# Kernel tuning notes

Measured on AMD Instinct MI355X. Metric: run time of the kernel, lower is better.

Reference implementation:

```python
import jax, jax.numpy as jnp
import numpy as np

N_QUBITS = 6
DIM = 2 ** N_QUBITS  # 64
Q_LAYERS = 2
CHUNK = 16

# ---- single-qubit rotation gate matrices (batched over leading dim) ----

def _rx(t):
    c = jnp.cos(t / 2).astype(jnp.complex64)
    s = jnp.sin(t / 2).astype(jnp.complex64)
    return jnp.stack([jnp.stack([c, -1j * s], -1), jnp.stack([-1j * s, c], -1)], -2)

def _ry(t):
    c = jnp.cos(t / 2).astype(jnp.complex64)
    s = jnp.sin(t / 2).astype(jnp.complex64)
    return jnp.stack([jnp.stack([c, -s], -1), jnp.stack([s, c], -1)], -2)

def _rz(t):
    e = jnp.exp(-0.5j * t.astype(jnp.complex64))
    z = jnp.zeros_like(e)
    return jnp.stack([jnp.stack([e, z], -1), jnp.stack([z, jnp.conj(e)], -1)], -2)


def _apply_1q(state, gate, wire):
    # state: (B, 64) complex64; gate: (B,2,2). PennyLane wire 0 = most-significant bit.
    dl, dr = 2 ** wire, 2 ** (N_QUBITS - 1 - wire)
    s = state.reshape(-1, dl, 2, dr)
    s = jnp.einsum('bkj,bljr->blkr', gate, s)
    return s.reshape(-1, DIM)


def _apply_crx(state, theta, control, target):
    s = state.reshape((-1,) + (2,) * N_QUBITS)
    s = jnp.moveaxis(s, (control + 1, target + 1), (1, 2))
    g = _rx(theta)  # (B,2,2)
    s1 = jnp.einsum('bkj,bj...->bk...', g, s[:, 1])
    s = jnp.concatenate([s[:, :1], s1[:, None]], axis=1)
    s = jnp.moveaxis(s, (1, 2), (control + 1, target + 1))
    return s.reshape(-1, DIM)


def _ansatz(state, params, n_layers):
    # unified ansatz: per layer, RX/RY/RZ on each qubit, ring of CRX forward, ring of CRX backward
    idx = 0
    for _ in range(n_layers):
        for i in range(N_QUBITS):
            state = _apply_1q(state, _rx(params[:, idx]), i)
            state = _apply_1q(state, _ry(params[:, idx + 1]), i)
            state = _apply_1q(state, _rz(params[:, idx + 2]), i)
            idx += 3
        for i in range(N_QUBITS):
            state = _apply_crx(state, params[:, idx], i, (i + 1) % N_QUBITS)
            idx += 1
        for i in range(N_QUBITS - 1, -1, -1):
            state = _apply_crx(state, params[:, idx], i, (i - 1) % N_QUBITS)
            idx += 1
    return state


_PX = jnp.array([[0, 1], [1, 0]], jnp.complex64)
_PY = jnp.array([[0, -1j], [1j, 0]], jnp.complex64)
_PZ = jnp.array([[1, 0], [0, -1]], jnp.complex64)


def _expvals(state):
    # expectations of X_i, Y_i, Z_i for all qubits -> (B, 3*n_qubits)
    outs = []
    B = state.shape[0]
    for P in (_PX, _PY, _PZ):
        g = jnp.broadcast_to(P, (B, 2, 2))
        for i in range(N_QUBITS):
            ps = _apply_1q(state, g, i)
            outs.append(jnp.sum(jnp.conj(state) * ps, axis=1).real)
    return jnp.stack(outs, axis=1).astype(jnp.float32)


def _forward(x, emb_w, emb_b, att_w1, att_b1, att_w2, att_b2, proj_w, proj_b,
             mix_re, mix_im, qff_params, out_w, out_b, ln_g, ln_b,
             cls_w1, cls_b1, cls_w2, cls_b2):
    B, C, T = x.shape
    # classical feature extractor: (B,C,T) -> (B,T,D)
    feats = jnp.einsum('bct,cd->btd', x, emb_w) + emb_b
    D = feats.shape[-1]
    n_chunks = T // CHUNK
    xc = feats.reshape(B, n_chunks, CHUNK, D)
    # attention-weighted chunk aggregation
    h = jnp.tanh(xc @ att_w1 + att_b1)
    scores = h @ att_w2 + att_b2                      # (B,nc,CHUNK,1)
    w = jax.nn.softmax(scores, axis=2)
    chunks = jnp.sum(w * xc, axis=2)                  # (B,nc,D)
    # quantum attention core: per-chunk ansatz params
    params = jax.nn.sigmoid(chunks @ proj_w + proj_b)  # (B,nc,60)
    flat = params.reshape(B * n_chunks, -1)
    state0 = jnp.zeros((B * n_chunks, DIM), jnp.complex64).at[:, 0].set(1.0)
    evolved = _ansatz(state0, flat, Q_LAYERS).reshape(B, n_chunks, DIM)
    # LCU mixing
    coeffs = (mix_re + 1j * mix_im).astype(jnp.complex64)
    coeffs = coeffs / (jnp.abs(coeffs).sum() + 1e-8)
    mixed = jnp.einsum('bti,t->bi', evolved, coeffs)
    norms = jnp.linalg.norm(mixed, axis=1, keepdims=True)
    mixed = mixed / (norms + 1e-9)
    # quantum feed-forward (shared params) + multi-observable measurement
    qp = jnp.broadcast_to(qff_params, (B, qff_params.shape[0]))
    qstate = _ansatz(mixed, qp, 1)
    qfeat = _expvals(qstate)                          # (B,18)
    out = qfeat @ out_w + out_b                       # (B,D)
    # LayerNorm
    mu = out.mean(-1, keepdims=True)
    var = out.var(-1, keepdims=True)
    out = (out - mu) / jnp.sqrt(var + 1e-5) * ln_g + ln_b
    # classifier head
    h2 = jax.nn.relu(out @ cls_w1 + cls_b1)
    return h2 @ cls_w2 + cls_b2


def setup_inputs() -> dict:
    key = jax.random.key(0)
    ks = jax.random.split(key, 20)
    B, C, T, D = 128, 64, 2048, 256
    NC = T // CHUNK        # 128 chunks
    NCP = 5 * N_QUBITS * Q_LAYERS  # 60 circuit params
    def nrm(k, shape, scale=0.05):
        return jax.random.normal(k, shape, jnp.float32) * scale
    return {
        'x': jax.random.normal(ks[0], (B, C, T), jnp.float32),
        'emb_w': nrm(ks[1], (C, D)), 'emb_b': nrm(ks[2], (D,)),
        'att_w1': nrm(ks[3], (D, D // 2)), 'att_b1': nrm(ks[4], (D // 2,)),
        'att_w2': nrm(ks[5], (D // 2, 1)), 'att_b2': nrm(ks[6], (1,)),
        'proj_w': nrm(ks[7], (D, NCP)), 'proj_b': nrm(ks[8], (NCP,)),
        'mix_re': jax.random.uniform(ks[9], (NC,), jnp.float32),
        'mix_im': jax.random.uniform(ks[10], (NC,), jnp.float32),
        'qff_params': nrm(ks[11], (5 * N_QUBITS,), 0.1),
        'out_w': nrm(ks[12], (3 * N_QUBITS, D)), 'out_b': nrm(ks[13], (D,)),
        'ln_g': jnp.ones((D,), jnp.float32), 'ln_b': jnp.zeros((D,), jnp.float32),
        'cls_w1': nrm(ks[14], (D, D)), 'cls_b1': nrm(ks[15], (D,)),
        'cls_w2': nrm(ks[16], (D, 2)), 'cls_b2': nrm(ks[17], (2,)),
    }


def reference(x, emb_w, emb_b, att_w1, att_b1, att_w2, att_b2, proj_w, proj_b,
              mix_re, mix_im, qff_params, out_w, out_b, ln_g, ln_b,
              cls_w1, cls_b1, cls_w2, cls_b2):
    return _forward(x, emb_w, emb_b, att_w1, att_b1, att_w2, att_b2, proj_w, proj_b,
                    mix_re, mix_im, qff_params, out_w, out_b, ln_g, ln_b,
                    cls_w1, cls_b1, cls_w2, cls_b2)
```

## Files before the change

### kernel.cpp

```cpp
#include <hip/hip_runtime.h>
#include <math.h>

#define NQ    6
#define QDIM  64
#define BB    128
#define CC    64
#define TT    2048
#define DD    256
#define NCH   128
#define CHLEN 16
#define HH    128
#define NCP   60

typedef __bf16 bf16x8 __attribute__((ext_vector_type(8)));
typedef float  f32x4  __attribute__((ext_vector_type(4)));

__device__ __forceinline__ float fast_tanh(float x) {
  float e = __expf(2.f * x);
  return 1.f - 2.f / (e + 1.f);
}

__device__ __forceinline__ float wave_sum(float v) {
#pragma unroll
  for (int off = 32; off >= 1; off >>= 1) v += __shfl_xor(v, off, 64);
  return v;
}

__device__ __forceinline__ void g_rx(float& re, float& im, int lane, int m, float half) {
  float c = __cosf(half), s = __sinf(half);
  float pre = __shfl_xor(re, m, 64);
  float pim = __shfl_xor(im, m, 64);
  float nre = c * re + s * pim;
  float nim = c * im - s * pre;
  re = nre; im = nim;
}
__device__ __forceinline__ void g_ry(float& re, float& im, int lane, int m, float half) {
  float c = __cosf(half), s = __sinf(half);
  float pre = __shfl_xor(re, m, 64);
  float pim = __shfl_xor(im, m, 64);
  float sg = (lane & m) ? s : -s;
  re = c * re + sg * pre;
  im = c * im + sg * pim;
}
__device__ __forceinline__ void g_rz(float& re, float& im, int lane, int m, float half) {
  float c = __cosf(half), s = __sinf(half);
  float sg = (lane & m) ? s : -s;
  float nre = c * re - sg * im;
  float nim = c * im + sg * re;
  re = nre; im = nim;
}
__device__ __forceinline__ void g_crx(float& re, float& im, int lane, int mc, int mt, float half) {
  float c = __cosf(half), s = __sinf(half);
  float pre = __shfl_xor(re, mt, 64);
  float pim = __shfl_xor(im, mt, 64);
  if (lane & mc) {
    float nre = c * re + s * pim;
    float nim = c * im - s * pre;
    re = nre; im = nim;
  }
}
__device__ __forceinline__ void ansatz_layer(float& re, float& im, int lane,
                                             const float* p) {
#pragma unroll
  for (int q = 0; q < 6; ++q) {
    int m = 1 << (5 - q);
    g_rx(re, im, lane, m, 0.5f * p[3 * q + 0]);
    g_ry(re, im, lane, m, 0.5f * p[3 * q + 1]);
    g_rz(re, im, lane, m, 0.5f * p[3 * q + 2]);
  }
#pragma unroll
  for (int q = 0; q < 6; ++q)
    g_crx(re, im, lane, 1 << (5 - q), 1 << (5 - ((q + 1) % 6)), 0.5f * p[18 + q]);
#pragma unroll
  for (int q = 5; q >= 0; --q)
    g_crx(re, im, lane, 1 << (5 - q), 1 << (5 - ((q + 5) % 6)), 0.5f * p[24 + (5 - q)]);
}

__global__ __launch_bounds__(256) void k0_prep(
    const float* __restrict__ emb_w, const float* __restrict__ emb_b,
    const float* __restrict__ att_w1, const float* __restrict__ att_b1,
    const float* __restrict__ proj_w, const float* __restrict__ proj_b,
    __bf16* __restrict__ WfH, __bf16* __restrict__ WfL,
    __bf16* __restrict__ PfH, __bf16* __restrict__ PfL,
    float* __restrict__ b_fused, float* __restrict__ pb_fused) {
  int idx = blockIdx.x * 256 + threadIdx.x;
  if (idx < 65536) {
    int out = idx >> 3, part = idx & 7;
    int j = out & 127, k = out >> 7;
    int d0 = part * 32;
    float a = 0.f;
#pragma unroll 8
    for (int d = d0; d < d0 + 32; ++d)
      a = fmaf(emb_w[k * 256 + d], att_w1[d * 128 + j], a);
    a += __shfl_xor(a, 1, 64); a += __shfl_xor(a, 2, 64); a += __shfl_xor(a, 4, 64);
    if (part == 0) {
      __bf16 h = (__bf16)a;
      WfH[j * 64 + k] = h; WfL[j * 64 + k] = (__bf16)(a - (float)h);
    }
  } else if (idx < 98304) {
    int i2 = idx - 65536;
    int out = i2 >> 3, part = i2 & 7;
    int n = out & 63, k = out >> 6;
    float a = 0.f;
    if (n < 60) {
      int d0 = part * 32;
#pragma unroll 8
      for (int d = d0; d < d0 + 32; ++d)
        a = fmaf(emb_w[k * 256 + d], proj_w[d * 60 + n], a);
    }
    a += __shfl_xor(a, 1, 64); a += __shfl_xor(a, 2, 64); a += __shfl_xor(a, 4, 64);
    if (part == 0) {
      __bf16 h = (__bf16)a;
      PfH[n * 64 + k] = h; PfL[n * 64 + k] = (__bf16)(a - (float)h);
    }
  } else if (idx < 99328) {
    int i3 = idx - 98304;
    int out = i3 >> 3, part = i3 & 7;
    float a = (part == 0) ? att_b1[out] : 0.f;
    int d0 = part * 32;
#pragma unroll 8
    for (int d = d0; d < d0 + 32; ++d)
      a = fmaf(emb_b[d], att_w1[d * 128 + out], a);
    a += __shfl_xor(a, 1, 64); a += __shfl_xor(a, 2, 64); a += __shfl_xor(a, 4, 64);
    if (part == 0) b_fused[out] = a;
  } else if (idx < 99840) {
    int i4 = idx - 99328;
    int out = i4 >> 3, part = i4 & 7;
    float a = 0.f;
    if (out < 60) {
      if (part == 0) a = proj_b[out];
      int d0 = part * 32;
#pragma unroll 8
      for (int d = d0; d < d0 + 32; ++d)
        a = fmaf(emb_b[d], proj_w[d * 60 + out], a);
    }
    a += __shfl_xor(a, 1, 64); a += __shfl_xor(a, 2, 64); a += __shfl_xor(a, 4, 64);
    if (part == 0) pb_fused[out] = a;
  }
}

__global__ __launch_bounds__(256) void k1_fused(
    const float* __restrict__ x, const float* __restrict__ att_w2,
    const __bf16* __restrict__ WfH, const __bf16* __restrict__ WfL,
    const __bf16* __restrict__ PfH, const __bf16* __restrict__ PfL,
    const float* __restrict__ b_fused, const float* __restrict__ pb_fused,
    float2* __restrict__ evolved) {
  const int blk = blockIdx.x;
  const int b = blk >> 5, cq = blk & 31;
  const int tid = threadIdx.x, wv = tid >> 6, lane = tid & 63;
  const int l15 = lane & 15, quad = lane >> 4;

  __shared__ float xtile[64][68];
  __shared__ float scoreS[4][64];
  __shared__ float4 uniF4[1024];
  char* uni = (char*)uniF4;
  bf16x8* afH = (bf16x8*)uni;
  bf16x8* afL = (bf16x8*)(uni + 8192);
  float*  wSm     = (float*)uni;
  __bf16* axH     = (__bf16*)(uni + 256);
  __bf16* axL     = (__bf16*)(uni + 768);
  float*  paramsS = (float*)(uni + 1280);
  float4* matS    = (float4*)(uni + 2240);
  float2* crxS    = (float2*)(uni + 5312);

  {
#pragma unroll
    for (int pass = 0; pass < 4; ++pass) {
      int k = pass * 16 + (tid >> 4), t4 = tid & 15;
      float4 v = *(const float4*)(x + ((size_t)(b * 64 + k)) * 2048 + cq * 64 + t4 * 4);
      xtile[t4 * 4 + 0][k] = v.x; xtile[t4 * 4 + 1][k] = v.y;
      xtile[t4 * 4 + 2][k] = v.z; xtile[t4 * 4 + 3][k] = v.w;
    }
  }
  __syncthreads();

  {
#pragma unroll
    for (int it = 0; it < 2; ++it) {
      int item = it * 256 + tid;
      int ln = item & 63, ks = (item >> 6) & 1, mt = item >> 7;
      const float* src = &xtile[mt * 16 + (ln & 15)][ks * 32 + (ln >> 4) * 8];
      float4 u0 = *(const float4*)src, u1 = *(const float4*)(src + 4);
      float vals[8] = {u0.x, u0.y, u0.z, u0.w, u1.x, u1.y, u1.z, u1.w};
      bf16x8 h, l;
#pragma unroll
      for (int j = 0; j < 8; ++j) {
        __bf16 hh = (__bf16)vals[j];
        h[j] = hh;
        l[j] = (__bf16)(vals[j] - (float)hh);
      }
      afH[(mt * 2 + ks) * 64 + ln] = h;
      afL[(mt * 2 + ks) * 64 + ln] = l;
    }
  }
  __syncthreads();

  f32x4 acc[4][2];
#pragma unroll
  for (int mt = 0; mt < 4; ++mt)
#pragma unroll
    for (int jt = 0; jt < 2; ++jt) acc[mt][jt] = (f32x4){0.f, 0.f, 0.f, 0.f};
#pragma unroll
  for (int ks = 0; ks < 2; ++ks) {
    bf16x8 ah[4], al[4];
#pragma unroll
    for (int mt = 0; mt < 4; ++mt) {
      ah[mt] = afH[(mt * 2 + ks) * 64 + lane];
      al[mt] = afL[(mt * 2 + ks) * 64 + lane];
    }
#pragma unroll
    for (int jt = 0; jt < 2; ++jt) {
      const size_t row = (size_t)(wv * 32 + jt * 16 + l15) * 64 + ks * 32 + 8 * quad;
      bf16x8 bh = *(const bf16x8*)(WfH + row);
      bf16x8 bl = *(const bf16x8*)(WfL + row);
#pragma unroll
      for (int mt = 0; mt < 4; ++mt) {
        acc[mt][jt] = __builtin_amdgcn_mfma_f32_16x16x32_bf16(ah[mt], bh, acc[mt][jt], 0, 0, 0);
        acc[mt][jt] = __builtin_amdgcn_mfma_f32_16x16x32_bf16(al[mt], bh, acc[mt][jt], 0, 0, 0);
        acc[mt][jt] = __builtin_amdgcn_mfma_f32_16x16x32_bf16(ah[mt], bl, acc[mt][jt], 0, 0, 0);
      }
    }
  }
  {
    float w2v[2], b1v[2];
#pragma unroll
    for (int jt = 0; jt < 2; ++jt) {
      int j = wv * 32 + jt * 16 + l15;
      w2v[jt] = att_w2[j];
      b1v[jt] = b_fused[j];
    }
#pragma unroll
    for (int mt = 0; mt < 4; ++mt)
#pragma unroll
      for (int r = 0; r < 4; ++r) {
        float sc = fast_tanh(acc[mt][0][r] + b1v[0]) * w2v[0] +
                   fast_tanh(acc[mt][1][r] + b1v[1]) * w2v[1];
        sc += __shfl_xor(sc, 1, 64);
        sc += __shfl_xor(sc, 2, 64);
        sc += __shfl_xor(sc, 4, 64);
        sc += __shfl_xor(sc, 8, 64);
        if (l15 == 0) scoreS[wv][mt * 16 + quad * 4 + r] = sc;
      }
  }
  __syncthreads();

  if (tid < 64) {
    const int c = tid >> 4, t = tid & 15, ct = c * 16 + t;
    float s = (scoreS[0][ct] + scoreS[1][ct]) + (scoreS[2][ct] + scoreS[3][ct]);
    float mx = s;
    mx = fmaxf(mx, __shfl_xor(mx, 1, 64));
    mx = fmaxf(mx, __shfl_xor(mx, 2, 64));
    mx = fmaxf(mx, __shfl_xor(mx, 4, 64));
    mx = fmaxf(mx, __shfl_xor(mx, 8, 64));
    float e = __expf(s - mx);
    float sum = e;
    sum += __shfl_xor(sum, 1, 64);
    sum += __shfl_xor(sum, 2, 64);
    sum += __shfl_xor(sum, 4, 64);
    sum += __shfl_xor(sum, 8, 64);
    wSm[ct] = e / sum;
  }
  __syncthreads();

  {
    const int c = wv, k = lane;
    float a = 0.f;
#pragma unroll
    for (int t = 0; t < 16; ++t) a = fmaf(wSm[c * 16 + t], xtile[c * 16 + t][k], a);
    __bf16 h = (__bf16)a;
    axH[c * 64 + k] = h;
    axL[c * 64 + k] = (__bf16)(a - (float)h);
  }
  __syncthreads();

  {
    const int jout = wv * 16 + l15;
    f32x4 acc3 = (f32x4){0.f, 0.f, 0.f, 0.f};
#pragma unroll
    for (int ks = 0; ks < 2; ++ks) {
      const size_t row = (size_t)jout * 64 + ks * 32 + 8 * quad;
      bf16x8 bh = *(const bf16x8*)(PfH + row);
      bf16x8 bl = *(const bf16x8*)(PfL + row);
      bf16x8 ax = (bf16x8)(__bf16)0.f, alx = (bf16x8)(__bf16)0.f;
      if (l15 < 4) {
        ax  = *(const bf16x8*)(axH + l15 * 64 + ks * 32 + 8 * quad);
        alx = *(const bf16x8*)(axL + l15 * 64 + ks * 32 + 8 * quad);
      }
      acc3 = __builtin_amdgcn_mfma_f32_16x16x32_bf16(ax, bh, acc3, 0, 0, 0);
      acc3 = __builtin_amdgcn_mfma_f32_16x16x32_bf16(alx, bh, acc3, 0, 0, 0);
      acc3 = __builtin_amdgcn_mfma_f32_16x16x32_bf16(ax, bl, acc3, 0, 0, 0);
    }
    if (jout < 60 && quad == 0) {
      float pbias = pb_fused[jout];
      const int layer = (jout >= 30) ? 1 : 0;
      const int pm = jout - layer * 30;
#pragma unroll
      for (int r = 0; r < 4; ++r) {
        float a = acc3[r] + pbias;
        float p = 1.f / (1.f + __expf(-a));
        paramsS[r * 60 + jout] = p;
        if (pm >= 18) {
          float sn, cs;
          __sincosf(0.5f * p, &sn, &cs);
          crxS[r * 24 + layer * 12 + (pm - 18)] = make_float2(cs, sn);
        }
      }
    }
  }
  __syncthreads();

  if (tid < 48) {
    const int r = tid / 12, g = tid % 12;
    const float* pp = paramsS + r * 60 + (g / 6) * 30 + (g % 6) * 3;
    float sa, ca, sb, cb, sg, cg;
    __sincosf(0.5f * pp[0], &sa, &ca);
    __sincosf(0.5f * pp[1], &sb, &cb);
    __sincosf(0.5f * pp[2], &sg, &cg);
    float m00r = cb * ca, m00i = sb * sa;
    float m01r = -sb * ca, m01i = -cb * sa;
    float m10r = sb * ca, m10i = -cb * sa;
    float m11r = cb * ca, m11i = -sb * sa;
    float4 b0, b1;
    b0.x = cg * m00r + sg * m00i;  b0.y = cg * m00i - sg * m00r;
    b0.z = cg * m01r + sg * m01i;  b0.w = cg * m01i - sg * m01r;
    b1.x = cg * m11r - sg * m11i;  b1.y = cg * m11i + sg * m11r;
    b1.z = cg * m10r - sg * m10i;  b1.w = cg * m10i + sg * m10r;
    matS[(r * 12 + g) * 2 + 0] = b0;
    matS[(r * 12 + g) * 2 + 1] = b1;
  }
  __syncthreads();

  {
    float re = (lane == 0) ? 1.f : 0.f, im = 0.f;
    const float4* mats = matS + wv * 24;
    const float2* crxs = crxS + wv * 24;
#pragma unroll
    for (int l = 0; l < 2; ++l) {
#pragma unroll
      for (int q = 0; q < 6; ++q) {
        const int m = 1 << (5 - q);
        float4 M = mats[(l * 6 + q) * 2 + ((lane & m) ? 1 : 0)];
        float pre = __shfl_xor(re, m, 64);
        float pim = __shfl_xor(im, m, 64);
        float nre = M.x * re - M.y * im + M.z * pre - M.w * pim;
        float nim = M.x * im + M.y * re + M.z * pim + M.w * pre;
        re = nre; im = nim;
      }
#pragma unroll
      for (int e = 0; e < 12; ++e) {
        const int q = (e < 6) ? e : (11 - e);
        const int mc = 1 << (5 - q);
        const int mt = (e < 6) ? (1 << (5 - ((q + 1) % 6)))
                               : (1 << (5 - ((q + 5) % 6)));
        float2 cs = crxs[l * 12 + e];
        float pre = __shfl_xor(re, mt, 64);
        float pim = __shfl_xor(im, mt, 64);
        float nre = fmaf(cs.y, pim, cs.x * re);
        float nim = fmaf(-cs.y, pre, cs.x * im);
        bool act = (lane & mc) != 0;
        re = act ? nre : re;
        im = act ? nim : im;
      }
    }
    evolved[((size_t)b * NCH + cq * 4 + wv) * QDIM + lane] = make_float2(re, im);
  }
}

__global__ __launch_bounds__(512) void k3_head(
    const float2* __restrict__ evolved, const float* __restrict__ mix_re,
    const float* __restrict__ mix_im, const float* __restrict__ qff,
    const float* __restrict__ out_w, const float* __restrict__ out_b,
    const float* __restrict__ ln_g, const float* __restrict__ ln_b,
    const float* __restrict__ cls_w1, const float* __restrict__ cls_b1,
    const float* __restrict__ cls_w2, const float* __restrict__ cls_b2,
    float* __restrict__ outp) {
  const int b = blockIdx.x, tid = threadIdx.x, wv = tid >> 6, lane = tid & 63;
  __shared__ float mreS[8][64], mimS[8][64];
  __shared__ float qfeatS[18];
  __shared__ float outS[DD];
  __shared__ float redS[8];
  __shared__ float clsR[2][DD];

  float are = 0.f, aim = 0.f;
#pragma unroll 4
  for (int t = wv * 16; t < wv * 16 + 16; ++t) {
    float2 e = evolved[((size_t)b * NCH + t) * QDIM + lane];
    float cr = mix_re[t], ci = mix_im[t];
    are = fmaf(cr, e.x, are); are = fmaf(-ci, e.y, are);
    aim = fmaf(cr, e.y, aim); aim = fmaf(ci, e.x, aim);
  }
  mreS[wv][lane] = are; mimS[wv][lane] = aim;
  __syncthreads();

  if (wv == 0) {
    float r0 = mix_re[lane], i0 = mix_im[lane];
    float r1 = mix_re[lane + 64], i1 = mix_im[lane + 64];
    float sp = sqrtf(r0 * r0 + i0 * i0) + sqrtf(r1 * r1 + i1 * i1);
    float S = wave_sum(sp) + 1e-8f;
    float re = 0.f, im = 0.f;
#pragma unroll
    for (int w = 0; w < 8; ++w) { re += mreS[w][lane]; im += mimS[w][lane]; }
    float invS = 1.f / S;
    re *= invS; im *= invS;
    float n2 = wave_sum(re * re + im * im);
    float scl = 1.f / (sqrtf(n2) + 1e-9f);
    re *= scl; im *= scl;
    float qp[30];
#pragma unroll
    for (int i = 0; i < 30; ++i) qp[i] = qff[i];
    ansatz_layer(re, im, lane, qp);
#pragma unroll
    for (int q = 0; q < 6; ++q) {
      int m = 1 << (5 - q);
      float pre = __shfl_xor(re, m, 64), pim = __shfl_xor(im, m, 64);
      float vx = re * pre + im * pim;
      float vy = (lane & m) ? (im * pre - re * pim) : (re * pim - im * pre);
      float vz = (lane & m) ? -(re * re + im * im) : (re * re + im * im);
      vx = wave_sum(vx); vy = wave_sum(vy); vz = wave_sum(vz);
      if (lane == 0) { qfeatS[q] = vx; qfeatS[6 + q] = vy; qfeatS[12 + q] = vz; }
    }
  }
  __syncthreads();

  float o = 0.f, dv = 0.f;
  if (tid < 256) {
    o = out_b[tid];
#pragma unroll
    for (int k = 0; k < 18; ++k) o = fmaf(qfeatS[k], out_w[k * DD + tid], o);
    float s1 = wave_sum(o);
    if (lane == 0) redS[wv] = s1;
  }
  __syncthreads();
  float mu = (redS[0] + redS[1] + redS[2] + redS[3]) * (1.f / 256.f);
  if (tid < 256) {
    dv = o - mu;
    float s2 = wave_sum(dv * dv);
    if (lane == 0) redS[wv] = s2;
  }
  __syncthreads();
  float var = (redS[0] + redS[1] + redS[2] + redS[3]) * (1.f / 256.f);
  if (tid < 256) {
    outS[tid] = dv / sqrtf(var + 1e-5f) * ln_g[tid] + ln_b[tid];
  }
  __syncthreads();

  {
    const int dd = tid & 255, hh = tid >> 8;
    float r = (hh == 0) ? cls_b1[dd] : 0.f;
#pragma unroll 8
    for (int d = hh * 128; d < hh * 128 + 128; ++d)
      r = fmaf(outS[d], cls_w1[(size_t)d * DD + dd], r);
    clsR[hh][dd] = r;
  }
  __syncthreads();
  if (tid < 256) {
    float r = fmaxf(clsR[0][tid] + clsR[1][tid], 0.f);
    float p0 = wave_sum(r * cls_w2[tid * 2 + 0]);
    float p1 = wave_sum(r * cls_w2[tid * 2 + 1]);
    if (lane == 0) { mreS[0][wv] = p0; mreS[1][wv] = p1; }
  }
  __syncthreads();
  if (tid == 0) {
    outp[b * 2 + 0] = (mreS[0][0] + mreS[0][1]) + (mreS[0][2] + mreS[0][3]) + cls_b2[0];
    outp[b * 2 + 1] = (mreS[1][0] + mreS[1][1]) + (mreS[1][2] + mreS[1][3]) + cls_b2[1];
  }
}

extern "C" void kernel_launch(void* const* d_in, const int* in_sizes, int n_in,
                              void* d_out, int out_size, void* d_ws, size_t ws_size,
                              hipStream_t stream) {
  const float* x      = (const float*)d_in[0];
  const float* emb_w  = (const float*)d_in[1];
  const float* emb_b  = (const float*)d_in[2];
  const float* att_w1 = (const float*)d_in[3];
  const float* att_b1 = (const float*)d_in[4];
  const float* att_w2 = (const float*)d_in[5];
  const float* proj_w = (const float*)d_in[7];
  const float* proj_b = (const float*)d_in[8];
  const float* mix_re = (const float*)d_in[9];
  const float* mix_im = (const float*)d_in[10];
  const float* qff    = (const float*)d_in[11];
  const float* out_w  = (const float*)d_in[12];
  const float* out_b  = (const float*)d_in[13];
  const float* ln_g   = (const float*)d_in[14];
  const float* ln_b   = (const float*)d_in[15];
  const float* cls_w1 = (const float*)d_in[16];
  const float* cls_b1 = (const float*)d_in[17];
  const float* cls_w2 = (const float*)d_in[18];
  const float* cls_b2 = (const float*)d_in[19];

  char* ws = (char*)d_ws;
  float2* evolved = (float2*)ws;
  size_t off = 8388608;
  __bf16* WfH = (__bf16*)(ws + off); off += 16384;
  __bf16* WfL = (__bf16*)(ws + off); off += 16384;
  __bf16* PfH = (__bf16*)(ws + off); off += 8192;
  __bf16* PfL = (__bf16*)(ws + off); off += 8192;
  float* b_fused  = (float*)(ws + off); off += 512;
  float* pb_fused = (float*)(ws + off); off += 256;

  k0_prep<<<390, 256, 0, stream>>>(emb_w, emb_b, att_w1, att_b1, proj_w, proj_b,
                                   WfH, WfL, PfH, PfL, b_fused, pb_fused);
  k1_fused<<<BB * 32, 256, 0, stream>>>(
      x, att_w2, WfH, WfL, PfH, PfL, b_fused, pb_fused, evolved);
  k3_head<<<BB, 512, 0, stream>>>(evolved, mix_re, mix_im, qff, out_w, out_b,
                                  ln_g, ln_b, cls_w1, cls_b1, cls_w2, cls_b2,
                                  (float*)d_out);
}
```

Before: 203.9 us.

## Drop fp32 x tile, split bf16 directly from global, halve accumulator live range

```diff
diff --git a/kernel.cpp b/kernel.cpp
--- a/kernel.cpp
+++ b/kernel.cpp
@@ -14,6 +14,10 @@
 
 typedef __bf16 bf16x8 __attribute__((ext_vector_type(8)));
 typedef float  f32x4  __attribute__((ext_vector_type(4)));
+
+__device__ __forceinline__ unsigned short bfbits(__bf16 v) {
+  return __builtin_bit_cast(unsigned short, v);
+}
 
 __device__ __forceinline__ float fast_tanh(float x) {
   float e = __expf(2.f * x);
@@ -139,7 +143,7 @@
   }
 }
 
-__global__ __launch_bounds__(256) void k1_fused(
+__global__ __launch_bounds__(256, 8) void k1_fused(
     const float* __restrict__ x, const float* __restrict__ att_w2,
     const __bf16* __restrict__ WfH, const __bf16* __restrict__ WfL,
     const __bf16* __restrict__ PfH, const __bf16* __restrict__ PfL,
@@ -150,77 +154,47 @@
   const int tid = threadIdx.x, wv = tid >> 6, lane = tid & 63;
   const int l15 = lane & 15, quad = lane >> 4;
 
-  __shared__ float xtile[64][68];
+  __shared__ float4 uniF4[1024];
   __shared__ float scoreS[4][64];
-  __shared__ float4 uniF4[1024];
+  __shared__ float wSm[4][16];
+  __shared__ __align__(16) __bf16 axH[4][64];
+  __shared__ __align__(16) __bf16 axL[4][64];
   char* uni = (char*)uniF4;
   bf16x8* afH = (bf16x8*)uni;
   bf16x8* afL = (bf16x8*)(uni + 8192);
-  float*  wSm     = (float*)uni;
-  __bf16* axH     = (__bf16*)(uni + 256);
-  __bf16* axL     = (__bf16*)(uni + 768);
-  float*  paramsS = (float*)(uni + 1280);
-  float4* matS    = (float4*)(uni + 2240);
-  float2* crxS    = (float2*)(uni + 5312);
+  float*  paramsS = (float*)uni;
+  float4* matS    = (float4*)(uni + 960);
+  float2* crxS    = (float2*)(uni + 4032);
 
   {
-#pragma unroll
-    for (int pass = 0; pass < 4; ++pass) {
-      int k = pass * 16 + (tid >> 4), t4 = tid & 15;
-      float4 v = *(const float4*)(x + ((size_t)(b * 64 + k)) * 2048 + cq * 64 + t4 * 4);
-      xtile[t4 * 4 + 0][k] = v.x; xtile[t4 * 4 + 1][k] = v.y;
-      xtile[t4 * 4 + 2][k] = v.z; xtile[t4 * 4 + 3][k] = v.w;
-    }
-  }
-  __syncthreads();
-
-  {
-#pragma unroll
-    for (int it = 0; it < 2; ++it) {
-      int item = it * 256 + tid;
-      int ln = item & 63, ks = (item >> 6) & 1, mt = item >> 7;
-      const float* src = &xtile[mt * 16 + (ln & 15)][ks * 32 + (ln >> 4) * 8];
-      float4 u0 = *(const float4*)src, u1 = *(const float4*)(src + 4);
-      float vals[8] = {u0.x, u0.y, u0.z, u0.w, u1.x, u1.y, u1.z, u1.w};
-      bf16x8 h, l;
-#pragma unroll
-      for (int j = 0; j < 8; ++j) {
-        __bf16 hh = (__bf16)vals[j];
-        h[j] = hh;
-        l[j] = (__bf16)(vals[j] - (float)hh);
+    unsigned short* afHu = (unsigned short*)uni;
+    unsigned short* afLu = (unsigned short*)(uni + 8192);
+#pragma unroll
+    for (int p = 0; p < 2; ++p) {
+      int slot = p * 256 + tid;
+      int t4 = slot & 15, kp = slot >> 4;
+      int k0 = kp * 2;
+      const float* base = x + ((size_t)(b * 64 + k0)) * 2048 + cq * 64 + t4 * 4;
+      float4 v0 = *(const float4*)base;
+      float4 v1 = *(const float4*)(base + 2048);
+      int ks = k0 >> 5, colq = (k0 >> 3) & 3, e = k0 & 7;
+      float a0[4] = {v0.x, v0.y, v0.z, v0.w};
+      float a1[4] = {v1.x, v1.y, v1.z, v1.w};
+#pragma unroll
+      for (int dt = 0; dt < 4; ++dt) {
+        int t = t4 * 4 + dt;
+        int frag = (t >> 4) * 2 + ks;
+        int ln = (t & 15) + colq * 16;
+        int widx = frag * 512 + ln * 8 + e;
+        __bf16 h0 = (__bf16)a0[dt]; __bf16 l0 = (__bf16)(a0[dt] - (float)h0);
+        __bf16 h1 = (__bf16)a1[dt]; __bf16 l1 = (__bf16)(a1[dt] - (float)h1);
+        *(ushort2*)(afHu + widx) = make_ushort2(bfbits(h0), bfbits(h1));
+        *(ushort2*)(afLu + widx) = make_ushort2(bfbits(l0), bfbits(l1));
       }
-      afH[(mt * 2 + ks) * 64 + ln] = h;
-      afL[(mt * 2 + ks) * 64 + ln] = l;
-    }
-  }
-  __syncthreads();
-
-  f32x4 acc[4][2];
-#pragma unroll
-  for (int mt = 0; mt < 4; ++mt)
-#pragma unroll
-    for (int jt = 0; jt < 2; ++jt) acc[mt][jt] = (f32x4){0.f, 0.f, 0.f, 0.f};
-#pragma unroll
-  for (int ks = 0; ks < 2; ++ks) {
-    bf16x8 ah[4], al[4];
-#pragma unroll
-    for (int mt = 0; mt < 4; ++mt) {
-      ah[mt] = afH[(mt * 2 + ks) * 64 + lane];
-      al[mt] = afL[(mt * 2 + ks) * 64 + lane];
-    }
-#pragma unroll
-    for (int jt = 0; jt < 2; ++jt) {
-      const size_t row = (size_t)(wv * 32 + jt * 16 + l15) * 64 + ks * 32 + 8 * quad;
-      bf16x8 bh = *(const bf16x8*)(WfH + row);
-      bf16x8 bl = *(const bf16x8*)(WfL + row);
-#pragma unroll
-      for (int mt = 0; mt < 4; ++mt) {
-        acc[mt][jt] = __builtin_amdgcn_mfma_f32_16x16x32_bf16(ah[mt], bh, acc[mt][jt], 0, 0, 0);
-        acc[mt][jt] = __builtin_amdgcn_mfma_f32_16x16x32_bf16(al[mt], bh, acc[mt][jt], 0, 0, 0);
-        acc[mt][jt] = __builtin_amdgcn_mfma_f32_16x16x32_bf16(ah[mt], bl, acc[mt][jt], 0, 0, 0);
-      }
-    }
-  }
+    }
+  }
+  __syncthreads();
+
   {
     float w2v[2], b1v[2];
 #pragma unroll
@@ -230,17 +204,42 @@
       b1v[jt] = b_fused[j];
     }
 #pragma unroll
-    for (int mt = 0; mt < 4; ++mt)
-#pragma unroll
-      for (int r = 0; r < 4; ++r) {
-        float sc = fast_tanh(acc[mt][0][r] + b1v[0]) * w2v[0] +
-                   fast_tanh(acc[mt][1][r] + b1v[1]) * w2v[1];
-        sc += __shfl_xor(sc, 1, 64);
-        sc += __shfl_xor(sc, 2, 64);
-        sc += __shfl_xor(sc, 4, 64);
-        sc += __shfl_xor(sc, 8, 64);
-        if (l15 == 0) scoreS[wv][mt * 16 + quad * 4 + r] = sc;
-      }
+    for (int half = 0; half < 2; ++half) {
+      f32x4 acc[2][2];
+#pragma unroll
+      for (int a2 = 0; a2 < 2; ++a2)
+#pragma unroll
+        for (int c2 = 0; c2 < 2; ++c2) acc[a2][c2] = (f32x4){0.f, 0.f, 0.f, 0.f};
+#pragma unroll
+      for (int ks = 0; ks < 2; ++ks)
+#pragma unroll
+        for (int jt = 0; jt < 2; ++jt) {
+          const size_t row = (size_t)(wv * 32 + jt * 16 + l15) * 64 + ks * 32 + 8 * quad;
+          bf16x8 bh = *(const bf16x8*)(WfH + row);
+          bf16x8 bl = *(const bf16x8*)(WfL + row);
+#pragma unroll
+          for (int mtl = 0; mtl < 2; ++mtl) {
+            int frag = (half * 2 + mtl) * 2 + ks;
+            bf16x8 ah = afH[frag * 64 + lane];
+            bf16x8 al = afL[frag * 64 + lane];
+            acc[mtl][jt] = __builtin_amdgcn_mfma_f32_16x16x32_bf16(ah, bh, acc[mtl][jt], 0, 0, 0);
+            acc[mtl][jt] = __builtin_amdgcn_mfma_f32_16x16x32_bf16(al, bh, acc[mtl][jt], 0, 0, 0);
+            acc[mtl][jt] = __builtin_amdgcn_mfma_f32_16x16x32_bf16(ah, bl, acc[mtl][jt], 0, 0, 0);
+          }
+        }
+#pragma unroll
+      for (int mtl = 0; mtl < 2; ++mtl)
+#pragma unroll
+        for (int r = 0; r < 4; ++r) {
+          float sc = fast_tanh(acc[mtl][0][r] + b1v[0]) * w2v[0] +
+                     fast_tanh(acc[mtl][1][r] + b1v[1]) * w2v[1];
+          sc += __shfl_xor(sc, 1, 64);
+          sc += __shfl_xor(sc, 2, 64);
+          sc += __shfl_xor(sc, 4, 64);
+          sc += __shfl_xor(sc, 8, 64);
+          if (l15 == 0) scoreS[wv][(half * 2 + mtl) * 16 + quad * 4 + r] = sc;
+        }
+    }
   }
   __syncthreads();
 
@@ -258,18 +257,39 @@
     sum += __shfl_xor(sum, 2, 64);
     sum += __shfl_xor(sum, 4, 64);
     sum += __shfl_xor(sum, 8, 64);
-    wSm[ct] = e / sum;
+    wSm[c][t] = e / sum;
   }
   __syncthreads();
 
   {
-    const int c = wv, k = lane;
-    float a = 0.f;
-#pragma unroll
-    for (int t = 0; t < 16; ++t) a = fmaf(wSm[c * 16 + t], xtile[c * 16 + t][k], a);
-    __bf16 h = (__bf16)a;
-    axH[c * 64 + k] = h;
-    axL[c * 64 + k] = (__bf16)(a - (float)h);
+    float wgt = wSm[wv][l15];
+#pragma unroll
+    for (int ks = 0; ks < 2; ++ks) {
+      bf16x8 h8 = afH[(wv * 2 + ks) * 64 + lane];
+      bf16x8 l8 = afL[(wv * 2 + ks) * 64 + lane];
+      float part[8];
+#pragma unroll
+      for (int e = 0; e < 8; ++e) part[e] = wgt * ((float)h8[e] + (float)l8[e]);
+#pragma unroll
+      for (int off = 1; off <= 8; off <<= 1)
+#pragma unroll
+        for (int e = 0; e < 8; ++e) part[e] += __shfl_xor(part[e], off, 64);
+      int kbase = ks * 32 + quad * 8;
+      if (l15 == 0) {
+        bf16x8 H;
+#pragma unroll
+        for (int e = 0; e < 8; ++e) H[e] = (__bf16)part[e];
+        *(bf16x8*)(&axH[wv][kbase]) = H;
+      } else if (l15 == 1) {
+        bf16x8 L;
+#pragma unroll
+        for (int e = 0; e < 8; ++e) {
+          __bf16 hh = (__bf16)part[e];
+          L[e] = (__bf16)(part[e] - (float)hh);
+        }
+        *(bf16x8*)(&axL[wv][kbase]) = L;
+      }
+    }
   }
   __syncthreads();
 
@@ -283,8 +303,8 @@
       bf16x8 bl = *(const bf16x8*)(PfL + row);
       bf16x8 ax = (bf16x8)(__bf16)0.f, alx = (bf16x8)(__bf16)0.f;
       if (l15 < 4) {
-        ax  = *(const bf16x8*)(axH + l15 * 64 + ks * 32 + 8 * quad);
-        alx = *(const bf16x8*)(axL + l15 * 64 + ks * 32 + 8 * quad);
+        ax  = *(const bf16x8*)(&axH[0][0] + l15 * 64 + ks * 32 + 8 * quad);
+        alx = *(const bf16x8*)(&axL[0][0] + l15 * 64 + ks * 32 + 8 * quad);
       }
       acc3 = __builtin_amdgcn_mfma_f32_16x16x32_bf16(ax, bh, acc3, 0, 0, 0);
       acc3 = __builtin_amdgcn_mfma_f32_16x16x32_bf16(alx, bh, acc3, 0, 0, 0);
```

Result: slower. 209.0 us (+2.5%).

## Give each wavefront one full chunk and drop block-level shared memory and barriers

Applied to the files above, without the earlier changes.

```diff
diff --git a/kernel.cpp b/kernel.cpp
--- a/kernel.cpp
+++ b/kernel.cpp
@@ -145,173 +145,131 @@
     const __bf16* __restrict__ PfH, const __bf16* __restrict__ PfL,
     const float* __restrict__ b_fused, const float* __restrict__ pb_fused,
     float2* __restrict__ evolved) {
-  const int blk = blockIdx.x;
-  const int b = blk >> 5, cq = blk & 31;
   const int tid = threadIdx.x, wv = tid >> 6, lane = tid & 63;
+  const int gc = blockIdx.x * 4 + wv;
+  const int b = gc >> 7, ch = gc & 127;
   const int l15 = lane & 15, quad = lane >> 4;
 
-  __shared__ float xtile[64][68];
-  __shared__ float scoreS[4][64];
-  __shared__ float4 uniF4[1024];
-  char* uni = (char*)uniF4;
-  bf16x8* afH = (bf16x8*)uni;
-  bf16x8* afL = (bf16x8*)(uni + 8192);
-  float*  wSm     = (float*)uni;
-  __bf16* axH     = (__bf16*)(uni + 256);
-  __bf16* axL     = (__bf16*)(uni + 768);
-  float*  paramsS = (float*)(uni + 1280);
-  float4* matS    = (float4*)(uni + 2240);
-  float2* crxS    = (float2*)(uni + 5312);
-
+  __shared__ float  pS[4][64];
+  __shared__ float4 matS[4][24];
+  __shared__ float2 crxS[4][24];
+
+  bf16x8 ahH[2], ahL[2];
   {
-#pragma unroll
-    for (int pass = 0; pass < 4; ++pass) {
-      int k = pass * 16 + (tid >> 4), t4 = tid & 15;
-      float4 v = *(const float4*)(x + ((size_t)(b * 64 + k)) * 2048 + cq * 64 + t4 * 4);
-      xtile[t4 * 4 + 0][k] = v.x; xtile[t4 * 4 + 1][k] = v.y;
-      xtile[t4 * 4 + 2][k] = v.z; xtile[t4 * 4 + 3][k] = v.w;
-    }
-  }
-  __syncthreads();
-
-  {
-#pragma unroll
-    for (int it = 0; it < 2; ++it) {
-      int item = it * 256 + tid;
-      int ln = item & 63, ks = (item >> 6) & 1, mt = item >> 7;
-      const float* src = &xtile[mt * 16 + (ln & 15)][ks * 32 + (ln >> 4) * 8];
-      float4 u0 = *(const float4*)src, u1 = *(const float4*)(src + 4);
-      float vals[8] = {u0.x, u0.y, u0.z, u0.w, u1.x, u1.y, u1.z, u1.w};
-      bf16x8 h, l;
+    const float* xbase = x + (size_t)(b * 64) * 2048 + ch * 16 + l15;
+#pragma unroll
+    for (int ks = 0; ks < 2; ++ks) {
+      float v[8];
+#pragma unroll
+      for (int j = 0; j < 8; ++j)
+        v[j] = xbase[(size_t)(ks * 32 + quad * 8 + j) * 2048];
 #pragma unroll
       for (int j = 0; j < 8; ++j) {
-        __bf16 hh = (__bf16)vals[j];
-        h[j] = hh;
-        l[j] = (__bf16)(vals[j] - (float)hh);
+        __bf16 h = (__bf16)v[j];
+        ahH[ks][j] = h;
+        ahL[ks][j] = (__bf16)(v[j] - (float)h);
       }
-      afH[(mt * 2 + ks) * 64 + ln] = h;
-      afL[(mt * 2 + ks) * 64 + ln] = l;
-    }
-  }
-  __syncthreads();
-
-  f32x4 acc[4][2];
-#pragma unroll
-  for (int mt = 0; mt < 4; ++mt)
-#pragma unroll
-    for (int jt = 0; jt < 2; ++jt) acc[mt][jt] = (f32x4){0.f, 0.f, 0.f, 0.f};
-#pragma unroll
-  for (int ks = 0; ks < 2; ++ks) {
-    bf16x8 ah[4], al[4];
-#pragma unroll
-    for (int mt = 0; mt < 4; ++mt) {
-      ah[mt] = afH[(mt * 2 + ks) * 64 + lane];
-      al[mt] = afL[(mt * 2 + ks) * 64 + lane];
-    }
-#pragma unroll
-    for (int jt = 0; jt < 2; ++jt) {
-      const size_t row = (size_t)(wv * 32 + jt * 16 + l15) * 64 + ks * 32 + 8 * quad;
+    }
+  }
+
+  float sc[4] = {0.f, 0.f, 0.f, 0.f};
+#pragma unroll
+  for (int jt = 0; jt < 8; ++jt) {
+    f32x4 acc = (f32x4){0.f, 0.f, 0.f, 0.f};
+#pragma unroll
+    for (int ks = 0; ks < 2; ++ks) {
+      const size_t row = (size_t)(jt * 16 + l15) * 64 + ks * 32 + 8 * quad;
       bf16x8 bh = *(const bf16x8*)(WfH + row);
       bf16x8 bl = *(const bf16x8*)(WfL + row);
-#pragma unroll
-      for (int mt = 0; mt < 4; ++mt) {
-        acc[mt][jt] = __builtin_amdgcn_mfma_f32_16x16x32_bf16(ah[mt], bh, acc[mt][jt], 0, 0, 0);
-        acc[mt][jt] = __builtin_amdgcn_mfma_f32_16x16x32_bf16(al[mt], bh, acc[mt][jt], 0, 0, 0);
-        acc[mt][jt] = __builtin_amdgcn_mfma_f32_16x16x32_bf16(ah[mt], bl, acc[mt][jt], 0, 0, 0);
-      }
-    }
-  }
+      acc = __builtin_amdgcn_mfma_f32_16x16x32_bf16(ahH[ks], bh, acc, 0, 0, 0);
+      acc = __builtin_amdgcn_mfma_f32_16x16x32_bf16(ahL[ks], bh, acc, 0, 0, 0);
+      acc = __builtin_amdgcn_mfma_f32_16x16x32_bf16(ahH[ks], bl, acc, 0, 0, 0);
+    }
+    const int j = jt * 16 + l15;
+    float w2v = att_w2[j], b1v = b_fused[j];
+#pragma unroll
+    for (int r = 0; r < 4; ++r)
+      sc[r] += fast_tanh(acc[r] + b1v) * w2v;
+  }
+#pragma unroll
+  for (int off = 1; off <= 8; off <<= 1)
+#pragma unroll
+    for (int r = 0; r < 4; ++r) sc[r] += __shfl_xor(sc[r], off, 64);
+
+  float w[4];
   {
-    float w2v[2], b1v[2];
-#pragma unroll
-    for (int jt = 0; jt < 2; ++jt) {
-      int j = wv * 32 + jt * 16 + l15;
-      w2v[jt] = att_w2[j];
-      b1v[jt] = b_fused[j];
-    }
-#pragma unroll
-    for (int mt = 0; mt < 4; ++mt)
-#pragma unroll
-      for (int r = 0; r < 4; ++r) {
-        float sc = fast_tanh(acc[mt][0][r] + b1v[0]) * w2v[0] +
-                   fast_tanh(acc[mt][1][r] + b1v[1]) * w2v[1];
-        sc += __shfl_xor(sc, 1, 64);
-        sc += __shfl_xor(sc, 2, 64);
-        sc += __shfl_xor(sc, 4, 64);
-        sc += __shfl_xor(sc, 8, 64);
-        if (l15 == 0) scoreS[wv][mt * 16 + quad * 4 + r] = sc;
-      }
-  }
-  __syncthreads();
-
-  if (tid < 64) {
-    const int c = tid >> 4, t = tid & 15, ct = c * 16 + t;
-    float s = (scoreS[0][ct] + scoreS[1][ct]) + (scoreS[2][ct] + scoreS[3][ct]);
-    float mx = s;
-    mx = fmaxf(mx, __shfl_xor(mx, 1, 64));
-    mx = fmaxf(mx, __shfl_xor(mx, 2, 64));
-    mx = fmaxf(mx, __shfl_xor(mx, 4, 64));
-    mx = fmaxf(mx, __shfl_xor(mx, 8, 64));
-    float e = __expf(s - mx);
-    float sum = e;
-    sum += __shfl_xor(sum, 1, 64);
-    sum += __shfl_xor(sum, 2, 64);
-    sum += __shfl_xor(sum, 4, 64);
-    sum += __shfl_xor(sum, 8, 64);
-    wSm[ct] = e / sum;
-  }
-  __syncthreads();
-
-  {
-    const int c = wv, k = lane;
-    float a = 0.f;
-#pragma unroll
-    for (int t = 0; t < 16; ++t) a = fmaf(wSm[c * 16 + t], xtile[c * 16 + t][k], a);
-    __bf16 h = (__bf16)a;
-    axH[c * 64 + k] = h;
-    axL[c * 64 + k] = (__bf16)(a - (float)h);
-  }
-  __syncthreads();
-
-  {
-    const int jout = wv * 16 + l15;
-    f32x4 acc3 = (f32x4){0.f, 0.f, 0.f, 0.f};
+    float mx = fmaxf(fmaxf(sc[0], sc[1]), fmaxf(sc[2], sc[3]));
+    mx = fmaxf(mx, __shfl_xor(mx, 16, 64));
+    mx = fmaxf(mx, __shfl_xor(mx, 32, 64));
+    float ssum = 0.f;
+#pragma unroll
+    for (int r = 0; r < 4; ++r) { w[r] = __expf(sc[r] - mx); ssum += w[r]; }
+    ssum += __shfl_xor(ssum, 16, 64);
+    ssum += __shfl_xor(ssum, 32, 64);
+#pragma unroll
+    for (int r = 0; r < 4; ++r) w[r] = w[r] / ssum;
+  }
+  float wN = 0.f;
+#pragma unroll
+  for (int r = 0; r < 4; ++r) {
+    float tmp = __shfl(w[r], (l15 >> 2) * 16, 64);
+    if ((l15 & 3) == r) wN = tmp;
+  }
+
+  bf16x8 axH[2], axL[2];
+#pragma unroll
+  for (int ks = 0; ks < 2; ++ks) {
+    float part[8];
+#pragma unroll
+    for (int e = 0; e < 8; ++e)
+      part[e] = wN * ((float)ahH[ks][e] + (float)ahL[ks][e]);
+#pragma unroll
+    for (int off = 1; off <= 8; off <<= 1)
+#pragma unroll
+      for (int e = 0; e < 8; ++e) part[e] += __shfl_xor(part[e], off, 64);
+#pragma unroll
+    for (int e = 0; e < 8; ++e) {
+      __bf16 h = (__bf16)part[e];
+      axH[ks][e] = h;
+      axL[ks][e] = (__bf16)(part[e] - (float)h);
+    }
+  }
+
+  float pv[4];
+#pragma unroll
+  for (int nt = 0; nt < 4; ++nt) {
+    f32x4 accp = (f32x4){0.f, 0.f, 0.f, 0.f};
 #pragma unroll
     for (int ks = 0; ks < 2; ++ks) {
-      const size_t row = (size_t)jout * 64 + ks * 32 + 8 * quad;
+      const size_t row = (size_t)(nt * 16 + l15) * 64 + ks * 32 + 8 * quad;
       bf16x8 bh = *(const bf16x8*)(PfH + row);
       bf16x8 bl = *(const bf16x8*)(PfL + row);
-      bf16x8 ax = (bf16x8)(__bf16)0.f, alx = (bf16x8)(__bf16)0.f;
-      if (l15 < 4) {
-        ax  = *(const bf16x8*)(axH + l15 * 64 + ks * 32 + 8 * quad);
-        alx = *(const bf16x8*)(axL + l15 * 64 + ks * 32 + 8 * quad);
-      }
-      acc3 = __builtin_amdgcn_mfma_f32_16x16x32_bf16(ax, bh, acc3, 0, 0, 0);
-      acc3 = __builtin_amdgcn_mfma_f32_16x16x32_bf16(alx, bh, acc3, 0, 0, 0);
-      acc3 = __builtin_amdgcn_mfma_f32_16x16x32_bf16(ax, bl, acc3, 0, 0, 0);
-    }
-    if (jout < 60 && quad == 0) {
-      float pbias = pb_fused[jout];
-      const int layer = (jout >= 30) ? 1 : 0;
-      const int pm = jout - layer * 30;
-#pragma unroll
-      for (int r = 0; r < 4; ++r) {
-        float a = acc3[r] + pbias;
-        float p = 1.f / (1.f + __expf(-a));
-        paramsS[r * 60 + jout] = p;
-        if (pm >= 18) {
-          float sn, cs;
-          __sincosf(0.5f * p, &sn, &cs);
-          crxS[r * 24 + layer * 12 + (pm - 18)] = make_float2(cs, sn);
-        }
-      }
-    }
-  }
-  __syncthreads();
-
-  if (tid < 48) {
-    const int r = tid / 12, g = tid % 12;
-    const float* pp = paramsS + r * 60 + (g / 6) * 30 + (g % 6) * 3;
+      accp = __builtin_amdgcn_mfma_f32_16x16x32_bf16(axH[ks], bh, accp, 0, 0, 0);
+      accp = __builtin_amdgcn_mfma_f32_16x16x32_bf16(axL[ks], bh, accp, 0, 0, 0);
+      accp = __builtin_amdgcn_mfma_f32_16x16x32_bf16(axH[ks], bl, accp, 0, 0, 0);
+    }
+    float a = accp[0] + pb_fused[nt * 16 + l15];
+    pv[nt] = 1.f / (1.f + __expf(-a));
+  }
+
+  if (quad == 0) {
+#pragma unroll
+    for (int nt = 0; nt < 4; ++nt) pS[wv][nt * 16 + l15] = pv[nt];
+    if (l15 >= 2 && l15 <= 13) {
+      float sn, cs;
+      __sincosf(0.5f * pv[1], &sn, &cs);
+      crxS[wv][l15 - 2] = make_float2(cs, sn);
+    }
+    if (l15 < 12) {
+      float sn, cs;
+      __sincosf(0.5f * pv[3], &sn, &cs);
+      crxS[wv][12 + l15] = make_float2(cs, sn);
+    }
+  }
+  asm volatile("s_waitcnt lgkmcnt(0)" ::: "memory");
+  if (quad == 1 && l15 < 12) {
+    const int g = l15, layer = g / 6, q = g % 6;
+    const float* pp = &pS[wv][layer * 30 + q * 3];
     float sa, ca, sb, cb, sg, cg;
     __sincosf(0.5f * pp[0], &sa, &ca);
     __sincosf(0.5f * pp[1], &sb, &cb);
@@ -325,15 +283,15 @@
     b0.z = cg * m01r + sg * m01i;  b0.w = cg * m01i - sg * m01r;
     b1.x = cg * m11r - sg * m11i;  b1.y = cg * m11i + sg * m11r;
     b1.z = cg * m10r - sg * m10i;  b1.w = cg * m10i + sg * m10r;
-    matS[(r * 12 + g) * 2 + 0] = b0;
-    matS[(r * 12 + g) * 2 + 1] = b1;
-  }
-  __syncthreads();
+    matS[wv][g * 2 + 0] = b0;
+    matS[wv][g * 2 + 1] = b1;
+  }
+  asm volatile("s_waitcnt lgkmcnt(0)" ::: "memory");
 
   {
     float re = (lane == 0) ? 1.f : 0.f, im = 0.f;
-    const float4* mats = matS + wv * 24;
-    const float2* crxs = crxS + wv * 24;
+    const float4* mats = &matS[wv][0];
+    const float2* crxs = &crxS[wv][0];
 #pragma unroll
     for (int l = 0; l < 2; ++l) {
 #pragma unroll
@@ -362,7 +320,7 @@
         im = act ? nim : im;
       }
     }
-    evolved[((size_t)b * NCH + cq * 4 + wv) * QDIM + lane] = make_float2(re, im);
+    evolved[((size_t)b * NCH + ch) * QDIM + lane] = make_float2(re, im);
   }
 }
 
```

Result: slower. 242.3 us (+18.8%).
